# Kernel optimization log

Measured on AMD Instinct MI355X. Metric: run time of the kernel, lower is better.

## Reference

```python
import jax, jax.numpy as jnp
import numpy as np

N_HEAD = 12

def setup_inputs() -> dict:
    key = jax.random.key(0)
    k1, k2, k3 = jax.random.split(key, 3)
    B, T, C = 8, 1024, 768
    x = jax.random.normal(k1, (B, T, C), dtype=jnp.float32)
    # torch nn.Linear weight layout: [out_features, in_features]
    W_attn = jax.random.normal(k2, (3 * C, C), dtype=jnp.float32) * 0.02
    b_attn = jax.random.normal(k3, (3 * C,), dtype=jnp.float32) * 0.02
    return {"x": x, "W_attn": W_attn, "b_attn": b_attn}

def reference(x, W_attn, b_attn):
    B, T, C = x.shape
    H = N_HEAD
    hs = C // H
    scale = 1.0 / jnp.sqrt(jnp.asarray(hs, x.dtype))
    # fused qkv projection: x @ W^T + b  -> [B, T, 3C]
    qkv = jnp.einsum('btc,oc->bto', x, W_attn) + b_attn
    qkv = qkv.reshape(B, T, 3, H, hs).transpose(2, 0, 3, 1, 4)  # [3, B, H, T, hs]
    q, k, v = qkv[0], qkv[1], qkv[2]
    scores = jnp.einsum('bhqd,bhkd->bhqk', q, k) * scale  # [B, H, T, T]
    causal = jnp.tril(jnp.ones((T, T), dtype=bool))
    # masked_fill(-inf) followed by ReLU == zero out masked positions after ReLU
    att = jnp.where(causal, jax.nn.relu(scores), jnp.zeros((), scores.dtype))
    y = jnp.einsum('bhqk,bhkd->bhqd', att, v)  # [B, H, T, hs]
    return y.transpose(0, 2, 1, 3).reshape(B, T, C)
```

## Files before the change

### kernel.cpp

```cpp
#include <hip/hip_runtime.h>
#include <hip/hip_bf16.h>
#include <stdint.h>

#define T_ 1024
#define C_ 768
#define H_ 12
#define HS 64

typedef __attribute__((ext_vector_type(8))) short bf16x8;
typedef __attribute__((ext_vector_type(4))) float f32x4;
typedef __attribute__((ext_vector_type(16))) float f32x16;

#define GLOAD16(g, l) __builtin_amdgcn_global_load_lds( \
    (const __attribute__((address_space(1))) uint32_t*)(g), \
    (__attribute__((address_space(3))) uint32_t*)(l), 16, 0, 0)

#define WAITCNT_VM(n) asm volatile("s_waitcnt vmcnt(" #n ")" ::: "memory")

__device__ __forceinline__ ushort f2b(float f) {
  uint32_t u = __builtin_bit_cast(uint32_t, f);
  u = (u + 0x7fffu + ((u >> 16) & 1u)) >> 16;
  return (ushort)u;
}

__device__ __forceinline__ uint cvtpk(float a, float b) {
  uint r;
  asm("v_cvt_pk_bf16_f32 %0, %1, %2" : "=v"(r) : "v"(a), "v"(b));
  return r;
}

__global__ __launch_bounds__(256) void cvt_bf16(
    const float* __restrict__ x, const float* __restrict__ wt,
    ushort* __restrict__ xb, ushort* __restrict__ wb) {
  const int NX4 = 8192 * 768 / 4;
  const int NW4 = 2304 * 768 / 4;
  int i = blockIdx.x * 256 + threadIdx.x;
  int stride = gridDim.x * 256;
  for (int idx = i; idx < NX4; idx += stride) {
    float4 f = ((const float4*)x)[idx];
    ushort4 o;
    o.x = f2b(f.x); o.y = f2b(f.y); o.z = f2b(f.z); o.w = f2b(f.w);
    ((ushort4*)xb)[idx] = o;
  }
  for (int idx = i; idx < NW4; idx += stride) {
    float4 f = ((const float4*)wt)[idx];
    ushort4 o;
    o.x = f2b(f.x); o.y = f2b(f.y); o.z = f2b(f.z); o.w = f2b(f.w);
    ((ushort4*)wb)[idx] = o;
  }
}

__global__ __launch_bounds__(256, 2) void qkv_gemm(
    const ushort* __restrict__ xb, const ushort* __restrict__ wb,
    const float* __restrict__ bias,
    ushort* __restrict__ qo, ushort* __restrict__ ko, ushort* __restrict__ vT) {
  __shared__ __align__(16) char smem[65536];
  const int tid = threadIdx.x, lane = tid & 63, w = tid >> 6;
  const int g = lane >> 4, l15 = lane & 15;
  const int id = blockIdx.x;
  const int wg = (id & 7) * 144 + (id >> 3);
  const int m0 = (wg / 18) * 128, n0 = (wg % 18) * 128;
  const int wr = w >> 1, wc = w & 1;
  f32x4 acc[4][4] = {};

  const ushort* sA[2];
  const ushort* sB[2];
  int sdst[2];
  #pragma unroll
  for (int c = 0; c < 2; ++c) {
    int i = c * 256 + tid, r = i >> 2, s = i & 3;
    int sc = (s ^ ((r >> 1) & 3)) * 8;
    sA[c] = xb + (size_t)(m0 + r) * 768 + sc;
    sB[c] = wb + (size_t)(n0 + r) * 768 + sc;
    sdst[c] = i * 16;
  }

#define STAGE(bufp_, kd, t) do { \
    _Pragma("unroll") \
    for (int c_ = 0; c_ < 2; ++c_) { \
      GLOAD16(sA[c_] + (t) * 64 + (kd) * 32, (bufp_) + (kd) * 8192 + sdst[c_]); \
      GLOAD16(sB[c_] + (t) * 64 + (kd) * 32, (bufp_) + 16384 + (kd) * 8192 + sdst[c_]); \
    } \
  } while (0)

#define COMPUTE(bufp_, kd) do { \
    const char* Ab = (bufp_) + (kd) * 8192; \
    const char* Bb = Ab + 16384; \
    bf16x8 af[4], bfr[4]; \
    _Pragma("unroll") \
    for (int mi = 0; mi < 4; ++mi) { \
      int r_ = wr * 64 + mi * 16 + l15; \
      af[mi] = *(const bf16x8*)(Ab + r_ * 64 + ((g ^ ((r_ >> 1) & 3)) << 4)); \
    } \
    _Pragma("unroll") \
    for (int ni = 0; ni < 4; ++ni) { \
      int r_ = wc * 64 + ni * 16 + l15; \
      bfr[ni] = *(const bf16x8*)(Bb + r_ * 64 + ((g ^ ((r_ >> 1) & 3)) << 4)); \
    } \
    __builtin_amdgcn_s_setprio(1); \
    _Pragma("unroll") \
    for (int mi = 0; mi < 4; ++mi) \
      _Pragma("unroll") \
      for (int ni = 0; ni < 4; ++ni) \
        acc[mi][ni] = __builtin_amdgcn_mfma_f32_16x16x32_bf16(af[mi], bfr[ni], acc[mi][ni], 0, 0, 0); \
    __builtin_amdgcn_s_setprio(0); \
  } while (0)

  STAGE(smem, 0, 0);
  STAGE(smem, 1, 0);
  #pragma unroll 2
  for (int t = 0; t < 12; ++t) {
    char* cur = smem + (t & 1) * 32768;
    char* nxt = smem + ((t + 1) & 1) * 32768;
    WAITCNT_VM(4);
    __builtin_amdgcn_s_barrier();
    if (t < 11) STAGE(nxt, 0, t + 1);
    COMPUTE(cur, 0);
    if (t < 11) { WAITCNT_VM(4); } else { WAITCNT_VM(0); }
    __builtin_amdgcn_s_barrier();
    if (t < 11) STAGE(nxt, 1, t + 1);
    COMPUTE(cur, 1);
  }
  __syncthreads();

  const int which = n0 / 768;
  if (which < 2) {
    ushort* outp = (which == 0) ? qo : ko;
    #pragma unroll
    for (int ni = 0; ni < 4; ++ni) {
      float bn = bias[n0 + wc * 64 + ni * 16 + l15];
      int nl = wc * 64 + ni * 16 + l15;
      #pragma unroll
      for (int mi = 0; mi < 4; ++mi) {
        #pragma unroll
        for (int r = 0; r < 4; ++r) {
          int ml = wr * 64 + mi * 16 + g * 4 + r;
          *(ushort*)(smem + ml * 256 + ((nl * 2) ^ ((ml & 7) << 4))) =
              f2b(acc[mi][ni][r] + bn);
        }
      }
    }
    __syncthreads();
    #pragma unroll
    for (int c = 0; c < 8; ++c) {
      int p = c * 256 + tid;
      int ml = p >> 4, nch = p & 15;
      uint4 val = *(const uint4*)(smem + ml * 256 + ((nch * 16) ^ ((ml & 7) << 4)));
      int m = m0 + ml;
      int nin = n0 + nch * 8 - which * 768;
      int h = nin >> 6, d = nin & 63;
      *(uint4*)(outp + ((size_t)((m >> 10) * H_ + h) * T_ + (m & (T_ - 1))) * HS + d) = val;
    }
  } else {
    #pragma unroll
    for (int ni = 0; ni < 4; ++ni) {
      float bn = bias[n0 + wc * 64 + ni * 16 + l15];
      int dl = wc * 64 + ni * 16 + l15;
      #pragma unroll
      for (int mi = 0; mi < 4; ++mi) {
        #pragma unroll
        for (int r = 0; r < 4; ++r) {
          int tl = wr * 64 + mi * 16 + g * 4 + r;
          *(ushort*)(smem + dl * 256 + ((tl * 2) ^ ((dl & 7) << 4))) =
              f2b(acc[mi][ni][r] + bn);
        }
      }
    }
    __syncthreads();
    const int b = m0 >> 10, t0base = m0 & 1023;
    #pragma unroll
    for (int c = 0; c < 8; ++c) {
      int p = c * 256 + tid;
      int dl = p >> 4, tch = p & 15;
      uint4 val = *(const uint4*)(smem + dl * 256 + ((tch * 16) ^ ((dl & 7) << 4)));
      int nin = n0 + dl - 1536;
      int h = nin >> 6, dd = nin & 63;
      *(uint4*)(vT + (((size_t)(b * H_ + h) * HS + dd) << 10) + t0base + tch * 8) = val;
    }
  }
}

__global__ __launch_bounds__(512, 4) void attn_relu(
    const ushort* __restrict__ q, const ushort* __restrict__ k,
    const ushort* __restrict__ vT, float* __restrict__ out) {
  __shared__ __align__(16) char smem[49152];
  const int tid = threadIdx.x, lane = tid & 63, w = tid >> 6;
  const int l31 = lane & 31, h = lane >> 5;
  const int raw = blockIdx.x;
  const int chunk = 3 - (raw / 96);
  const int bh = raw % 96;
  const size_t base = (size_t)bh * (T_ * HS);
  const int q0w = chunk * 256 + w * 32;
  const int nkt = chunk * 4 + 4;

  bf16x8 qf[4];
  #pragma unroll
  for (int s = 0; s < 4; ++s)
    qf[s] = *(const bf16x8*)(q + base + (size_t)(q0w + l31) * HS + s * 16 + h * 8);

  const int rowS = tid >> 3;
  const int colS = ((tid & 7) ^ (rowS & 7)) * 8;
  const int dstS = tid * 16;

#define STAGE_KV(bb_, kt) do { \
    GLOAD16(k  + base + (size_t)((kt) * 64 + rowS) * HS + colS, (bb_) + dstS); \
    GLOAD16(vT + base + (size_t)rowS * T_ + (kt) * 64 + colS, (bb_) + 8192 + dstS); \
  } while (0)

  f32x16 yacc0 = {}, yacc1 = {};

#define ATTN_TILE(cb_, kt) do { \
    const char* Kb = (cb_); \
    const char* Vb = (cb_) + 8192; \
    _Pragma("unroll") \
    for (int kr = 0; kr < 2; ++kr) { \
      int kbase = (kt) * 64 + kr * 32; \
      if (kbase <= q0w + 31) { \
        f32x16 sacc = {}; \
        int arow = kr * 32 + l31; \
        __builtin_amdgcn_s_setprio(1); \
        _Pragma("unroll") \
        for (int s = 0; s < 4; ++s) { \
          bf16x8 kf = *(const bf16x8*)(Kb + arow * 128 + (((2 * s + h) ^ (arow & 7)) << 4)); \
          sacc = __builtin_amdgcn_mfma_f32_32x32x16_bf16(kf, qf[s], sacc, 0, 0, 0); \
        } \
        __builtin_amdgcn_s_setprio(0); \
        const bool fullk = (kbase + 31 <= q0w); \
        uint wds[8]; \
        _Pragma("unroll") \
        for (int i = 0; i < 8; ++i) { \
          float a = fmaxf(sacc[2 * i] * 0.125f, 0.0f); \
          float b = fmaxf(sacc[2 * i + 1] * 0.125f, 0.0f); \
          if (!fullk) { \
            int r0 = 2 * i, r1 = 2 * i + 1; \
            if (kbase + (r0 & 3) + 8 * (r0 >> 2) + 4 * h > q0w + l31) a = 0.0f; \
            if (kbase + (r1 & 3) + 8 * (r1 >> 2) + 4 * h > q0w + l31) b = 0.0f; \
          } \
          wds[i] = cvtpk(a, b); \
        } \
        __builtin_amdgcn_s_setprio(1); \
        _Pragma("unroll") \
        for (int t = 0; t < 2; ++t) { \
          int4 pw = { (int)wds[4 * t], (int)wds[4 * t + 1], \
                      (int)wds[4 * t + 2], (int)wds[4 * t + 3] }; \
          bf16x8 pa = __builtin_bit_cast(bf16x8, pw); \
          _Pragma("unroll") \
          for (int dt = 0; dt < 2; ++dt) { \
            int d = dt * 32 + l31; \
            uint2 lo = *(const uint2*)(Vb + d * 128 + (((4 * kr + 2 * t) ^ (d & 7)) << 4) + 8 * h); \
            uint2 hi = *(const uint2*)(Vb + d * 128 + (((4 * kr + 2 * t + 1) ^ (d & 7)) << 4) + 8 * h); \
            int4 vv = { (int)lo.x, (int)lo.y, (int)hi.x, (int)hi.y }; \
            bf16x8 vf = __builtin_bit_cast(bf16x8, vv); \
            if (dt == 0) yacc0 = __builtin_amdgcn_mfma_f32_32x32x16_bf16(pa, vf, yacc0, 0, 0, 0); \
            else         yacc1 = __builtin_amdgcn_mfma_f32_32x32x16_bf16(pa, vf, yacc1, 0, 0, 0); \
          } \
        } \
        __builtin_amdgcn_s_setprio(0); \
      } \
    } \
  } while (0)

  STAGE_KV(smem, 0);
  if (nkt > 1) STAGE_KV(smem + 16384, 1);
  char* cptr = smem;
  char* sptr = smem + 32768;
  for (int kt = 0; kt < nkt - 1; ++kt) {
    WAITCNT_VM(2);
    __builtin_amdgcn_s_barrier();
    if (kt + 2 < nkt) STAGE_KV(sptr, kt + 2);
    ATTN_TILE(cptr, kt);
    cptr += 16384; if (cptr == smem + 49152) cptr = smem;
    sptr += 16384; if (sptr == smem + 49152) sptr = smem;
  }
  WAITCNT_VM(0);
  __builtin_amdgcn_s_barrier();
  ATTN_TILE(cptr, nkt - 1);

  const int bb = bh / H_, hh = bh % H_;
  #pragma unroll
  for (int r = 0; r < 16; ++r) {
    int qrow = q0w + (r & 3) + 8 * (r >> 2) + 4 * h;
    float* op = out + (size_t)(bb * T_ + qrow) * C_ + hh * HS;
    op[l31] = yacc0[r];
    op[32 + l31] = yacc1[r];
  }
}

extern "C" void kernel_launch(void* const* d_in, const int* in_sizes, int n_in,
                              void* d_out, int out_size, void* d_ws, size_t ws_size,
                              hipStream_t stream) {
  const float* x    = (const float*)d_in[0];
  const float* W    = (const float*)d_in[1];
  const float* bias = (const float*)d_in[2];
  float* out = (float*)d_out;

  char* ws = (char*)d_ws;
  ushort* xb = (ushort*)ws;
  ushort* wb = (ushort*)(ws + 12582912);
  ushort* qb = (ushort*)(ws + 16121856);
  ushort* kb = (ushort*)(ws + 28704768);
  ushort* vT = (ushort*)(ws + 41287680);

  cvt_bf16<<<2048, 256, 0, stream>>>(x, W, xb, wb);
  qkv_gemm<<<1152, 256, 0, stream>>>(xb, wb, bias, qb, kb, vT);
  attn_relu<<<384, 512, 0, stream>>>(qb, kb, vT, out);
}
```

Baseline: 150.7 us.

## Widen QKV GEMM tile to 128x256 and split attention K/V staging

The QKV projection GEMM now uses 512-thread blocks, each computing a 128x256 output tile. The A tile is shared across twice as many columns, which cuts redundant A loads and halves the grid, at the cost of 96KB of LDS per block and likely lower block occupancy per CU. The attention kernel replaces its triple-buffered combined K/V staging with separate double buffers for K and V. The next K tile is loaded during the QK phase and the next V tile during the PV phase, with the packed probabilities kept in registers between phases. This lowers LDS use to 32KB but shortens the prefetch distance to one tile.

```diff
diff --git a/kernel.cpp b/kernel.cpp
--- a/kernel.cpp
+++ b/kernel.cpp
@@ -50,42 +50,43 @@
   }
 }
 
-__global__ __launch_bounds__(256, 2) void qkv_gemm(
+__global__ __launch_bounds__(512, 2) void qkv_gemm(
     const ushort* __restrict__ xb, const ushort* __restrict__ wb,
     const float* __restrict__ bias,
     ushort* __restrict__ qo, ushort* __restrict__ ko, ushort* __restrict__ vT) {
-  __shared__ __align__(16) char smem[65536];
+  __shared__ __align__(16) char smem[98304];
   const int tid = threadIdx.x, lane = tid & 63, w = tid >> 6;
   const int g = lane >> 4, l15 = lane & 15;
   const int id = blockIdx.x;
-  const int wg = (id & 7) * 144 + (id >> 3);
-  const int m0 = (wg / 18) * 128, n0 = (wg % 18) * 128;
-  const int wr = w >> 1, wc = w & 1;
+  const int wg = (id & 7) * 72 + (id >> 3);
+  const int m0 = (wg / 9) * 128, n0 = (wg % 9) * 256;
+  const int wr = w >> 2, wc = w & 3;
   f32x4 acc[4][4] = {};
 
-  const ushort* sA[2];
+  const ushort* sA;
   const ushort* sB[2];
-  int sdst[2];
+  int dA, dB[2];
+  {
+    int r = tid >> 2, s = tid & 3;
+    sA = xb + (size_t)(m0 + r) * 768 + (s ^ ((r >> 1) & 3)) * 8;
+    dA = tid * 16;
+  }
   #pragma unroll
   for (int c = 0; c < 2; ++c) {
-    int i = c * 256 + tid, r = i >> 2, s = i & 3;
-    int sc = (s ^ ((r >> 1) & 3)) * 8;
-    sA[c] = xb + (size_t)(m0 + r) * 768 + sc;
-    sB[c] = wb + (size_t)(n0 + r) * 768 + sc;
-    sdst[c] = i * 16;
+    int i = c * 512 + tid, r = i >> 2, s = i & 3;
+    sB[c] = wb + (size_t)(n0 + r) * 768 + (s ^ ((r >> 1) & 3)) * 8;
+    dB[c] = i * 16;
   }
 
 #define STAGE(bufp_, kd, t) do { \
-    _Pragma("unroll") \
-    for (int c_ = 0; c_ < 2; ++c_) { \
-      GLOAD16(sA[c_] + (t) * 64 + (kd) * 32, (bufp_) + (kd) * 8192 + sdst[c_]); \
-      GLOAD16(sB[c_] + (t) * 64 + (kd) * 32, (bufp_) + 16384 + (kd) * 8192 + sdst[c_]); \
-    } \
+    GLOAD16(sA + (t) * 64 + (kd) * 32, (bufp_) + (kd) * 8192 + dA); \
+    GLOAD16(sB[0] + (t) * 64 + (kd) * 32, (bufp_) + 16384 + (kd) * 16384 + dB[0]); \
+    GLOAD16(sB[1] + (t) * 64 + (kd) * 32, (bufp_) + 16384 + (kd) * 16384 + dB[1]); \
   } while (0)
 
 #define COMPUTE(bufp_, kd) do { \
     const char* Ab = (bufp_) + (kd) * 8192; \
-    const char* Bb = Ab + 16384; \
+    const char* Bb = (bufp_) + 16384 + (kd) * 16384; \
     bf16x8 af[4], bfr[4]; \
     _Pragma("unroll") \
     for (int mi = 0; mi < 4; ++mi) { \
@@ -110,13 +111,13 @@
   STAGE(smem, 1, 0);
   #pragma unroll 2
   for (int t = 0; t < 12; ++t) {
-    char* cur = smem + (t & 1) * 32768;
-    char* nxt = smem + ((t + 1) & 1) * 32768;
-    WAITCNT_VM(4);
+    char* cur = smem + (t & 1) * 49152;
+    char* nxt = smem + ((t + 1) & 1) * 49152;
+    WAITCNT_VM(3);
     __builtin_amdgcn_s_barrier();
     if (t < 11) STAGE(nxt, 0, t + 1);
     COMPUTE(cur, 0);
-    if (t < 11) { WAITCNT_VM(4); } else { WAITCNT_VM(0); }
+    if (t < 11) { WAITCNT_VM(3); } else { WAITCNT_VM(0); }
     __builtin_amdgcn_s_barrier();
     if (t < 11) STAGE(nxt, 1, t + 1);
     COMPUTE(cur, 1);
@@ -128,14 +129,14 @@
     ushort* outp = (which == 0) ? qo : ko;
     #pragma unroll
     for (int ni = 0; ni < 4; ++ni) {
-      float bn = bias[n0 + wc * 64 + ni * 16 + l15];
       int nl = wc * 64 + ni * 16 + l15;
+      float bn = bias[n0 + nl];
       #pragma unroll
       for (int mi = 0; mi < 4; ++mi) {
         #pragma unroll
         for (int r = 0; r < 4; ++r) {
           int ml = wr * 64 + mi * 16 + g * 4 + r;
-          *(ushort*)(smem + ml * 256 + ((nl * 2) ^ ((ml & 7) << 4))) =
+          *(ushort*)(smem + ml * 512 + ((nl * 2) ^ ((ml & 7) << 4))) =
               f2b(acc[mi][ni][r] + bn);
         }
       }
@@ -143,9 +144,9 @@
     __syncthreads();
     #pragma unroll
     for (int c = 0; c < 8; ++c) {
-      int p = c * 256 + tid;
-      int ml = p >> 4, nch = p & 15;
-      uint4 val = *(const uint4*)(smem + ml * 256 + ((nch * 16) ^ ((ml & 7) << 4)));
+      int p = c * 512 + tid;
+      int ml = p >> 5, nch = p & 31;
+      uint4 val = *(const uint4*)(smem + ml * 512 + ((nch * 16) ^ ((ml & 7) << 4)));
       int m = m0 + ml;
       int nin = n0 + nch * 8 - which * 768;
       int h = nin >> 6, d = nin & 63;
@@ -154,8 +155,8 @@
   } else {
     #pragma unroll
     for (int ni = 0; ni < 4; ++ni) {
-      float bn = bias[n0 + wc * 64 + ni * 16 + l15];
       int dl = wc * 64 + ni * 16 + l15;
+      float bn = bias[n0 + dl];
       #pragma unroll
       for (int mi = 0; mi < 4; ++mi) {
         #pragma unroll
@@ -170,7 +171,7 @@
     const int b = m0 >> 10, t0base = m0 & 1023;
     #pragma unroll
     for (int c = 0; c < 8; ++c) {
-      int p = c * 256 + tid;
+      int p = c * 512 + tid;
       int dl = p >> 4, tch = p & 15;
       uint4 val = *(const uint4*)(smem + dl * 256 + ((tch * 16) ^ ((dl & 7) << 4)));
       int nin = n0 + dl - 1536;
@@ -183,7 +184,7 @@
 __global__ __launch_bounds__(512, 4) void attn_relu(
     const ushort* __restrict__ q, const ushort* __restrict__ k,
     const ushort* __restrict__ vT, float* __restrict__ out) {
-  __shared__ __align__(16) char smem[49152];
+  __shared__ __align__(16) char smem[32768];
   const int tid = threadIdx.x, lane = tid & 63, w = tid >> 6;
   const int l31 = lane & 31, h = lane >> 5;
   const int raw = blockIdx.x;
@@ -202,16 +203,15 @@
   const int colS = ((tid & 7) ^ (rowS & 7)) * 8;
   const int dstS = tid * 16;
 
-#define STAGE_KV(bb_, kt) do { \
-    GLOAD16(k  + base + (size_t)((kt) * 64 + rowS) * HS + colS, (bb_) + dstS); \
-    GLOAD16(vT + base + (size_t)rowS * T_ + (kt) * 64 + colS, (bb_) + 8192 + dstS); \
-  } while (0)
+#define STAGE_K(bb_, kt) \
+    GLOAD16(k + base + (size_t)((kt) * 64 + rowS) * HS + colS, (bb_) + dstS)
+#define STAGE_V(bb_, kt) \
+    GLOAD16(vT + base + (size_t)rowS * T_ + (kt) * 64 + colS, (bb_) + dstS)
 
   f32x16 yacc0 = {}, yacc1 = {};
-
-#define ATTN_TILE(cb_, kt) do { \
-    const char* Kb = (cb_); \
-    const char* Vb = (cb_) + 8192; \
+  uint wds[2][8];
+
+#define QK_PHASE(Kb_, kt) do { \
     _Pragma("unroll") \
     for (int kr = 0; kr < 2; ++kr) { \
       int kbase = (kt) * 64 + kr * 32; \
@@ -221,12 +221,11 @@
         __builtin_amdgcn_s_setprio(1); \
         _Pragma("unroll") \
         for (int s = 0; s < 4; ++s) { \
-          bf16x8 kf = *(const bf16x8*)(Kb + arow * 128 + (((2 * s + h) ^ (arow & 7)) << 4)); \
+          bf16x8 kf = *(const bf16x8*)((Kb_) + arow * 128 + (((2 * s + h) ^ (arow & 7)) << 4)); \
           sacc = __builtin_amdgcn_mfma_f32_32x32x16_bf16(kf, qf[s], sacc, 0, 0, 0); \
         } \
         __builtin_amdgcn_s_setprio(0); \
         const bool fullk = (kbase + 31 <= q0w); \
-        uint wds[8]; \
         _Pragma("unroll") \
         for (int i = 0; i < 8; ++i) { \
           float a = fmaxf(sacc[2 * i] * 0.125f, 0.0f); \
@@ -236,19 +235,28 @@
             if (kbase + (r0 & 3) + 8 * (r0 >> 2) + 4 * h > q0w + l31) a = 0.0f; \
             if (kbase + (r1 & 3) + 8 * (r1 >> 2) + 4 * h > q0w + l31) b = 0.0f; \
           } \
-          wds[i] = cvtpk(a, b); \
+          wds[kr][i] = cvtpk(a, b); \
         } \
+      } \
+    } \
+  } while (0)
+
+#define PV_PHASE(Vb_, kt) do { \
+    _Pragma("unroll") \
+    for (int kr = 0; kr < 2; ++kr) { \
+      int kbase = (kt) * 64 + kr * 32; \
+      if (kbase <= q0w + 31) { \
         __builtin_amdgcn_s_setprio(1); \
         _Pragma("unroll") \
         for (int t = 0; t < 2; ++t) { \
-          int4 pw = { (int)wds[4 * t], (int)wds[4 * t + 1], \
-                      (int)wds[4 * t + 2], (int)wds[4 * t + 3] }; \
+          int4 pw = { (int)wds[kr][4 * t], (int)wds[kr][4 * t + 1], \
+                      (int)wds[kr][4 * t + 2], (int)wds[kr][4 * t + 3] }; \
           bf16x8 pa = __builtin_bit_cast(bf16x8, pw); \
           _Pragma("unroll") \
           for (int dt = 0; dt < 2; ++dt) { \
             int d = dt * 32 + l31; \
-            uint2 lo = *(const uint2*)(Vb + d * 128 + (((4 * kr + 2 * t) ^ (d & 7)) << 4) + 8 * h); \
-            uint2 hi = *(const uint2*)(Vb + d * 128 + (((4 * kr + 2 * t + 1) ^ (d & 7)) << 4) + 8 * h); \
+            uint2 lo = *(const uint2*)((Vb_) + d * 128 + (((4 * kr + 2 * t) ^ (d & 7)) << 4) + 8 * h); \
+            uint2 hi = *(const uint2*)((Vb_) + d * 128 + (((4 * kr + 2 * t + 1) ^ (d & 7)) << 4) + 8 * h); \
             int4 vv = { (int)lo.x, (int)lo.y, (int)hi.x, (int)hi.y }; \
             bf16x8 vf = __builtin_bit_cast(bf16x8, vv); \
             if (dt == 0) yacc0 = __builtin_amdgcn_mfma_f32_32x32x16_bf16(pa, vf, yacc0, 0, 0, 0); \
@@ -260,21 +268,22 @@
     } \
   } while (0)
 
-  STAGE_KV(smem, 0);
-  if (nkt > 1) STAGE_KV(smem + 16384, 1);
-  char* cptr = smem;
-  char* sptr = smem + 32768;
-  for (int kt = 0; kt < nkt - 1; ++kt) {
-    WAITCNT_VM(2);
+  STAGE_K(smem, 0);
+  STAGE_V(smem + 16384, 0);
+  for (int kt = 0; kt < nkt; ++kt) {
+    const char* Kb = smem + (kt & 1) * 8192;
+    const char* Vb = smem + 16384 + (kt & 1) * 8192;
+    char* Kn = smem + ((kt + 1) & 1) * 8192;
+    char* Vn = smem + 16384 + ((kt + 1) & 1) * 8192;
+    WAITCNT_VM(1);
     __builtin_amdgcn_s_barrier();
-    if (kt + 2 < nkt) STAGE_KV(sptr, kt + 2);
-    ATTN_TILE(cptr, kt);
-    cptr += 16384; if (cptr == smem + 49152) cptr = smem;
-    sptr += 16384; if (sptr == smem + 49152) sptr = smem;
-  }
-  WAITCNT_VM(0);
-  __builtin_amdgcn_s_barrier();
-  ATTN_TILE(cptr, nkt - 1);
+    if (kt + 1 < nkt) STAGE_K(Kn, kt + 1);
+    QK_PHASE(Kb, kt);
+    if (kt + 1 < nkt) { WAITCNT_VM(1); } else { WAITCNT_VM(0); }
+    __builtin_amdgcn_s_barrier();
+    if (kt + 1 < nkt) STAGE_V(Vn, kt + 1);
+    PV_PHASE(Vb, kt);
+  }
 
   const int bb = bh / H_, hh = bh % H_;
   #pragma unroll
@@ -302,6 +311,6 @@
   ushort* vT = (ushort*)(ws + 41287680);
 
   cvt_bf16<<<2048, 256, 0, stream>>>(x, W, xb, wb);
-  qkv_gemm<<<1152, 256, 0, stream>>>(xb, wb, bias, qb, kb, vT);
+  qkv_gemm<<<576, 512, 0, stream>>>(xb, wb, bias, qb, kb, vT);
   attn_relu<<<384, 512, 0, stream>>>(qb, kb, vT, out);
 }
```

Measured after the change: 160.1 us. +6.2%, slower.
